# Optimization experiments

Measured on AMD Instinct MI355X. Metric: run time of the kernel, lower is better.

## Reference

```python
import jax, jax.numpy as jnp
import numpy as np

N_NODES = 100000
N_EDGES = 1600000
IN_DIM = 128
HEADS = 8
HEAD_DIM = 16  # output_dim 128 / heads 8
NEG_SLOPE = 0.2  # PyG GATConv default LeakyReLU slope


def setup_inputs() -> dict:
    key = jax.random.key(0)
    k1, k2, k3, k4, k5 = jax.random.split(key, 5)
    x = jax.random.normal(k1, (N_NODES, IN_DIM), dtype=jnp.float32)
    edge_index = jax.random.randint(k2, (2, N_EDGES), 0, N_NODES, dtype=jnp.int64)
    scale = 1.0 / np.sqrt(IN_DIM)
    W = jax.random.normal(k3, (IN_DIM, HEADS * HEAD_DIM), dtype=jnp.float32) * scale
    a_src = jax.random.normal(k4, (HEADS, HEAD_DIM), dtype=jnp.float32) * scale
    a_dst = jax.random.normal(k5, (HEADS, HEAD_DIM), dtype=jnp.float32) * scale
    bias = jnp.zeros((HEADS * HEAD_DIM,), dtype=jnp.float32)
    return {"x": x, "edge_index": edge_index, "W": W, "a_src": a_src, "a_dst": a_dst, "bias": bias}


def reference(x, edge_index, W, a_src, a_dst, bias):
    N = x.shape[0]
    H, D = a_src.shape
    # add self-loops (PyG GATConv default add_self_loops=True)
    loop = jnp.arange(N, dtype=edge_index.dtype)
    src = jnp.concatenate([edge_index[0], loop])  # message sources j
    dst = jnp.concatenate([edge_index[1], loop])  # message targets i

    h = (x @ W).reshape(N, H, D)  # per-head projected features
    alpha_src = jnp.sum(h * a_src, axis=-1)  # [N, H]
    alpha_dst = jnp.sum(h * a_dst, axis=-1)  # [N, H]

    # edge-wise attention logits, softmax over incoming edges of each dst node
    e = jax.nn.leaky_relu(alpha_src[src] + alpha_dst[dst], NEG_SLOPE)  # [E', H]
    e_max = jax.ops.segment_max(e, dst, num_segments=N)
    e_exp = jnp.exp(e - e_max[dst])
    denom = jax.ops.segment_sum(e_exp, dst, num_segments=N)
    alpha = e_exp / (denom[dst] + 1e-16)  # [E', H]

    # weighted scatter-sum of source features
    out = jax.ops.segment_sum(alpha[:, :, None] * h[src], dst, num_segments=N)  # [N, H, D]
    out = out.reshape(N, H * D) + bias
    # wrapper: ReLU (concat=True), dropout is identity in eval mode
    return jax.nn.relu(out)
```

## Files before the change

### kernel.cpp

```cpp
#include <hip/hip_runtime.h>
#include <hip/hip_bf16.h>

#define NEG_SLOPE 0.2f
#define NBUCK 782
#define ABLK 8192
#define CAP 3072

typedef __attribute__((ext_vector_type(8))) short bf16x8v;
typedef __attribute__((ext_vector_type(4))) float f32x4;
typedef __attribute__((ext_vector_type(2))) float f32x2;

__device__ __forceinline__ unsigned f2bf_bits(float f) {
    unsigned u = __float_as_uint(f);
    return (u + 0x7fffu + ((u >> 16) & 1u)) >> 16;
}
__device__ __forceinline__ float bflo(unsigned u) { return __uint_as_float(u << 16); }
__device__ __forceinline__ float bfhi(unsigned u) { return __uint_as_float(u & 0xffff0000u); }

__device__ __forceinline__ void pkfma(f32x2& a, f32x2 x, f32x2 w) {
    asm("v_pk_fma_f32 %0, %1, %2, %0" : "+v"(a) : "v"(x), "v"(w));
}

__global__ __launch_bounds__(256) void gemm_mfma(const float* __restrict__ x,
                                                 const short* __restrict__ WtE,
                                                 short* __restrict__ hout,
                                                 float* __restrict__ as,
                                                 float* __restrict__ ad, int N) {
    __shared__ short xs[64 * 136];
    __shared__ short wt[144 * 136];
    const int tid = threadIdx.x;
    const int r0 = blockIdx.x * 64;

#pragma unroll
    for (int p = 0; p < 9; ++p) {
        int idx = p * 256 + tid;
        int n = idx >> 4, kk = (idx & 15) * 8;
        *(uint4*)&wt[n * 136 + kk] = *(const uint4*)(WtE + n * 128 + kk);
    }
#pragma unroll
    for (int p = 0; p < 8; ++p) {
        int lin = p * 1024 + tid * 4;
        int row = lin >> 7, k = lin & 127;
        int gr = r0 + row;
        int grc = gr < N ? gr : N - 1;
        float4 v = *(const float4*)(x + (size_t)grc * 128 + k);
        unsigned p0 = f2bf_bits(v.x) | (f2bf_bits(v.y) << 16);
        unsigned p1 = f2bf_bits(v.z) | (f2bf_bits(v.w) << 16);
        *(uint2*)&xs[row * 136 + k] = make_uint2(p0, p1);
    }
    __syncthreads();

    const int wv = tid >> 6;
    const int lane = tid & 63;
    const int lc = lane & 15, quad = lane >> 4;
    f32x4 acc[9];
#pragma unroll
    for (int c = 0; c < 9; ++c) acc[c] = (f32x4){0.f, 0.f, 0.f, 0.f};
    const short* aB = &xs[(wv * 16 + lc) * 136 + quad * 8];
    const short* bB = &wt[lc * 136 + quad * 8];
#pragma unroll
    for (int kc = 0; kc < 4; ++kc) {
        bf16x8v af = *(const bf16x8v*)(aB + kc * 32);
#pragma unroll
        for (int c = 0; c < 9; ++c) {
            bf16x8v bf = *(const bf16x8v*)(bB + c * (16 * 136) + kc * 32);
            acc[c] = __builtin_amdgcn_mfma_f32_16x16x32_bf16(af, bf, acc[c], 0, 0, 0);
        }
    }

    const int rowb = r0 + wv * 16 + quad * 4;
#pragma unroll
    for (int c = 0; c < 8; ++c) {
#pragma unroll
        for (int r = 0; r < 4; ++r) {
            int row = rowb + r;
            if (row < N) hout[(size_t)row * 128 + c * 16 + lc] = (short)f2bf_bits(acc[c][r]);
        }
    }
#pragma unroll
    for (int r = 0; r < 4; ++r) {
        int row = rowb + r;
        if (row < N) {
            if (lc < 8) as[row * 8 + lc] = acc[8][r];
            else        ad[row * 8 + (lc - 8)] = acc[8][r];
        }
    }
}

__global__ __launch_bounds__(1024) void bucket_edges(const int* __restrict__ ei, int E,
                                                     int nblk,
                                                     unsigned* __restrict__ slab,
                                                     int2* __restrict__ csG,
                                                     const float* __restrict__ W,
                                                     const float* __restrict__ a_src,
                                                     const float* __restrict__ a_dst,
                                                     short* __restrict__ WtE) {
    const int t = threadIdx.x;
    const int blk = blockIdx.x;

    if (blk >= nblk) {
        int id = (blk - nblk) * 1024 + t;
        if (id < 144 * 128) {
            int n = id >> 7, k = id & 127;
            float v;
            if (n < 128) {
                v = W[k * 128 + n];
            } else if (n < 136) {
                int hh = n - 128; float s = 0.f;
#pragma unroll
                for (int d = 0; d < 16; ++d) s += W[k * 128 + hh * 16 + d] * a_src[hh * 16 + d];
                v = s;
            } else {
                int hh = n - 136; float s = 0.f;
#pragma unroll
                for (int d = 0; d < 16; ++d) s += W[k * 128 + hh * 16 + d] * a_dst[hh * 16 + d];
                v = s;
            }
            WtE[id] = (short)f2bf_bits(v);
        }
        return;
    }

    __shared__ int hist[1024];
    __shared__ int cur[NBUCK];
    __shared__ int wpart[16];
    const int base = blk * ABLK;
    int count = E - base; if (count > ABLK) count = ABLK;

    int sr[8], dr[8];
    hist[t] = 0;
#pragma unroll
    for (int k = 0; k < 8; ++k) {
        int i = k * 1024 + t;
        if (i < count) { sr[k] = ei[base + i]; dr[k] = ei[E + base + i]; }
    }
    __syncthreads();
#pragma unroll
    for (int k = 0; k < 8; ++k) {
        int i = k * 1024 + t;
        if (i < count) atomicAdd(&hist[dr[k] >> 7], 1);
    }
    __syncthreads();
    int v = hist[t];
    int lane = t & 63, wid = t >> 6;
    int sc = v;
#pragma unroll
    for (int off = 1; off < 64; off <<= 1) { int u = __shfl_up(sc, off); if (lane >= off) sc += u; }
    if (lane == 63) wpart[wid] = sc;
    __syncthreads();
    if (wid == 0 && lane < 16) {
        int wv = wpart[lane], wsum = wv;
#pragma unroll
        for (int off = 1; off < 16; off <<= 1) { int u = __shfl_up(wsum, off); if (lane >= off) wsum += u; }
        wpart[lane] = wsum - wv;
    }
    __syncthreads();
    int excl = sc - v + wpart[wid];
    if (t < NBUCK) {
        csG[(size_t)blk * NBUCK + t] = make_int2(v, excl);
        cur[t] = excl;
    }
    __syncthreads();
#pragma unroll
    for (int k = 0; k < 8; ++k) {
        int i = k * 1024 + t;
        if (i < count) {
            int d = dr[k];
            int pos = atomicAdd(&cur[d >> 7], 1);
            slab[(size_t)blk * ABLK + pos] = (unsigned)sr[k] | ((unsigned)(d & 127) << 17);
        }
    }
}

__global__ __launch_bounds__(512) void build_csr(const unsigned* __restrict__ slab,
                                                 const int2* __restrict__ csG,
                                                 int nblk, int N,
                                                 int* __restrict__ rowS,
                                                 int* __restrict__ rowE,
                                                 int* __restrict__ sortedSrc) {
    __shared__ int eL[CAP];
    __shared__ int incl[512];
    __shared__ int cS[512];
    __shared__ int stS[512];
    __shared__ int lp[128];
    __shared__ int wpart[8];
    __shared__ int halfSum;
    const int bb = blockIdx.x;
    const int t = threadIdx.x;
    const int nodeBase = bb << 7;
    const int bBase = bb * CAP;

    int c = 0, st = 0;
    if (t < nblk) { int2 cs = csG[(size_t)t * NBUCK + bb]; c = cs.x; st = cs.y; }
    cS[t] = c; stS[t] = st;
    if (t < 128) lp[t] = 0;
    int lane = t & 63, wid = t >> 6;
    int sc = c;
#pragma unroll
    for (int off = 1; off < 64; off <<= 1) { int u = __shfl_up(sc, off); if (lane >= off) sc += u; }
    if (lane == 63) wpart[wid] = sc;
    __syncthreads();
    if (wid == 0 && lane < 8) {
        int wv = wpart[lane], wsum = wv;
#pragma unroll
        for (int off = 1; off < 8; off <<= 1) { int u = __shfl_up(wsum, off); if (lane >= off) wsum += u; }
        wpart[lane] = wsum - wv;
    }
    __syncthreads();
    incl[t] = sc + wpart[wid];
    __syncthreads();
    int total = incl[511];
    if (total > CAP) total = CAP;
    {
        const int grp = t >> 3, li = t & 7;
        for (int s = grp; s < nblk; s += 64) {
            int cc = cS[s];
            int off0 = incl[s] - cc;
            const unsigned* p = slab + (size_t)s * ABLK + stS[s];
            for (int i = li; i < cc; i += 8) eL[off0 + i] = (int)p[i];
        }
    }
    __syncthreads();
    for (int e = t; e < total; e += 512) atomicAdd(&lp[((unsigned)eL[e]) >> 17], 1);
    __syncthreads();
    int cnt = 0, s2 = 0;
    if (t < 128) {
        cnt = lp[t];
        s2 = cnt;
#pragma unroll
        for (int off = 1; off < 64; off <<= 1) { int u = __shfl_up(s2, off); if (lane >= off) s2 += u; }
        if (t == 63) halfSum = s2;
    }
    __syncthreads();
    if (t < 128) {
        int inc2 = s2 + (t >= 64 ? halfSum : 0);
        int ex = inc2 - cnt;
        int gn = nodeBase + t;
        if (gn < N) { rowS[gn] = bBase + ex; rowE[gn] = bBase + ex + cnt; }
        lp[t] = ex;
    }
    __syncthreads();
    for (int e = t; e < total; e += 512) {
        unsigned pk = (unsigned)eL[e];
        int pos = atomicAdd(&lp[pk >> 17], 1);
        sortedSrc[bBase + pos] = (int)(pk & 0x1FFFFu);
    }
}

__global__ __launch_bounds__(256, 6) void aggregate(const int* __restrict__ rowS,
                                                    const int* __restrict__ rowE,
                                                    const int* __restrict__ sortedSrc,
                                                    const short* __restrict__ h,
                                                    const float* __restrict__ as,
                                                    const float* __restrict__ ad,
                                                    const float* __restrict__ bias,
                                                    float* __restrict__ out, int N) {
    const int wv = __builtin_amdgcn_readfirstlane((int)(threadIdx.x >> 6));
    const int node = blockIdx.x * 4 + wv;
    if (node >= N) return;
    const int lane = threadIdx.x & 63;
    const int g = lane >> 3, p = lane & 7;
    const int start = rowS[node], end = rowE[node];
    const float adv = ad[node * 8 + p];
    const short* hb = h + p * 16;

    f32x2 acc[8];
#pragma unroll
    for (int k = 0; k < 8; ++k) acc[k] = (f32x2){0.f, 0.f};
    float dsum = 0.f;

    float as0 = 0.f, as1 = 0.f, as2 = 0.f;
    uint4 hA0 = {0,0,0,0}, hA1 = {0,0,0,0};
    uint4 hB0 = {0,0,0,0}, hB1 = {0,0,0,0};
    uint4 hC0 = {0,0,0,0}, hC1 = {0,0,0,0};

#define SLOT_LOAD(EV, ASV, H0, H1)                                  \
    if ((EV) < end) {                                               \
        int j = sortedSrc[EV];                                      \
        ASV = as[j * 8 + p];                                        \
        const uint4* hp = (const uint4*)(hb + (size_t)j * 128);     \
        H0 = hp[0]; H1 = hp[1];                                     \
    }

#define EDGE_COMPUTE(ASV, H0, H1)                                   \
    {                                                               \
        float tt = ASV + adv;                                       \
        tt = tt > 0.f ? tt : NEG_SLOPE * tt;                        \
        float w = __expf(tt);                                       \
        f32x2 wp = {w, w};                                          \
        f32x2 tv;                                                   \
        tv.x = bflo(H0.x); tv.y = bfhi(H0.x); pkfma(acc[0], tv, wp); \
        tv.x = bflo(H0.y); tv.y = bfhi(H0.y); pkfma(acc[1], tv, wp); \
        tv.x = bflo(H0.z); tv.y = bfhi(H0.z); pkfma(acc[2], tv, wp); \
        tv.x = bflo(H0.w); tv.y = bfhi(H0.w); pkfma(acc[3], tv, wp); \
        tv.x = bflo(H1.x); tv.y = bfhi(H1.x); pkfma(acc[4], tv, wp); \
        tv.x = bflo(H1.y); tv.y = bfhi(H1.y); pkfma(acc[5], tv, wp); \
        tv.x = bflo(H1.z); tv.y = bfhi(H1.z); pkfma(acc[6], tv, wp); \
        tv.x = bflo(H1.w); tv.y = bfhi(H1.w); pkfma(acc[7], tv, wp); \
        dsum += w;                                                  \
    }

    int e = start + g;
    SLOT_LOAD(e, as0, hA0, hA1)
    SLOT_LOAD(e + 8, as1, hB0, hB1)
    SLOT_LOAD(e + 16, as2, hC0, hC1)

    if (end - start <= 24) {
        if (e < end)      EDGE_COMPUTE(as0, hA0, hA1)
        if (e + 8 < end)  EDGE_COMPUTE(as1, hB0, hB1)
        if (e + 16 < end) EDGE_COMPUTE(as2, hC0, hC1)
    } else {
        while (e < end) {
            EDGE_COMPUTE(as0, hA0, hA1)
            SLOT_LOAD(e + 24, as0, hA0, hA1)
            if (e + 8 < end) EDGE_COMPUTE(as1, hB0, hB1)
            SLOT_LOAD(e + 32, as1, hB0, hB1)
            if (e + 16 < end) EDGE_COMPUTE(as2, hC0, hC1)
            SLOT_LOAD(e + 40, as2, hC0, hC1)
            e += 24;
        }
    }

#pragma unroll
    for (int m = 8; m <= 32; m <<= 1) {
#pragma unroll
        for (int k = 0; k < 8; ++k) {
            acc[k].x += __shfl_xor(acc[k].x, m);
            acc[k].y += __shfl_xor(acc[k].y, m);
        }
        dsum += __shfl_xor(dsum, m);
    }
    {
        float slas = as[node * 8 + p];
        const uint4* hp = (const uint4*)(hb + (size_t)node * 128);
        uint4 s0 = hp[0], s1 = hp[1];
        EDGE_COMPUTE(slas, s0, s1)
    }
    if (g == 0) {
        float inv = 1.0f / (dsum + 1e-16f);
        float* op = out + (size_t)node * 128 + p * 16;
        const float* bp = bias + p * 16;
#pragma unroll
        for (int q = 0; q < 4; ++q) {
            float4 bv = *(const float4*)(bp + q * 4);
            float o0 = acc[2 * q].x     * inv + bv.x;
            float o1 = acc[2 * q].y     * inv + bv.y;
            float o2 = acc[2 * q + 1].x * inv + bv.z;
            float o3 = acc[2 * q + 1].y * inv + bv.w;
            o0 = o0 > 0.f ? o0 : 0.f; o1 = o1 > 0.f ? o1 : 0.f;
            o2 = o2 > 0.f ? o2 : 0.f; o3 = o3 > 0.f ? o3 : 0.f;
            *(float4*)(op + q * 4) = make_float4(o0, o1, o2, o3);
        }
    }
#undef SLOT_LOAD
#undef EDGE_COMPUTE
}

extern "C" void kernel_launch(void* const* d_in, const int* in_sizes, int n_in,
                              void* d_out, int out_size, void* d_ws, size_t ws_size,
                              hipStream_t stream) {
    const float* x     = (const float*)d_in[0];
    const int*   ei    = (const int*)d_in[1];
    const float* W     = (const float*)d_in[2];
    const float* a_src = (const float*)d_in[3];
    const float* a_dst = (const float*)d_in[4];
    const float* bias  = (const float*)d_in[5];
    float* out = (float*)d_out;

    const int N = in_sizes[0] / 128;
    const int E = in_sizes[1] / 2;
    const int nblk = (E + ABLK - 1) / ABLK;

    char* ws = (char*)d_ws;
    size_t off = 0;
    auto alloc = [&](size_t bytes) { void* p = ws + off; off = (off + bytes + 255) & ~(size_t)255; return p; };
    short*    h         = (short*)alloc((size_t)N * 128 * 2);
    float*    as        = (float*)alloc((size_t)N * 8 * 4);
    float*    ad        = (float*)alloc((size_t)N * 8 * 4);
    unsigned* slab      = (unsigned*)alloc((size_t)nblk * ABLK * 4);
    int2*     csG       = (int2*)alloc((size_t)nblk * NBUCK * 8);
    int*      sortedSrc = (int*)alloc((size_t)NBUCK * CAP * 4);
    int*      rowS      = (int*)alloc((size_t)N * 4);
    int*      rowE      = (int*)alloc((size_t)N * 4);
    short*    WtE       = (short*)alloc((size_t)144 * 128 * 2);

    bucket_edges<<<nblk + 18, 1024, 0, stream>>>(ei, E, nblk, slab, csG, W, a_src, a_dst, WtE);
    gemm_mfma<<<(N + 63) / 64, 256, 0, stream>>>(x, WtE, h, as, ad, N);
    build_csr<<<NBUCK, 512, 0, stream>>>(slab, csG, nblk, N, rowS, rowE, sortedSrc);
    aggregate<<<(N + 3) / 4, 256, 0, stream>>>(rowS, rowE, sortedSrc, h, as, ad, bias, out, N);
}
```

Measured before the change: 227.7 us.

## Assign one node per 8-lane group, degree-sorted within each bucket

```diff
diff --git a/kernel.cpp b/kernel.cpp
--- a/kernel.cpp
+++ b/kernel.cpp
@@ -177,12 +177,15 @@
                                                  int nblk, int N,
                                                  int* __restrict__ rowS,
                                                  int* __restrict__ rowE,
-                                                 int* __restrict__ sortedSrc) {
+                                                 int* __restrict__ sortedSrc,
+                                                 int* __restrict__ nodeOrd) {
     __shared__ int eL[CAP];
     __shared__ int incl[512];
     __shared__ int cS[512];
     __shared__ int stS[512];
     __shared__ int lp[128];
+    __shared__ int degS[128];
+    __shared__ int rnk[128];
     __shared__ int wpart[8];
     __shared__ int halfSum;
     const int bb = blockIdx.x;
@@ -193,7 +196,7 @@
     int c = 0, st = 0;
     if (t < nblk) { int2 cs = csG[(size_t)t * NBUCK + bb]; c = cs.x; st = cs.y; }
     cS[t] = c; stS[t] = st;
-    if (t < 128) lp[t] = 0;
+    if (t < 128) { lp[t] = 0; rnk[t] = 0; }
     int lane = t & 63, wid = t >> 6;
     int sc = c;
 #pragma unroll
@@ -226,6 +229,7 @@
     int cnt = 0, s2 = 0;
     if (t < 128) {
         cnt = lp[t];
+        degS[t] = cnt;
         s2 = cnt;
 #pragma unroll
         for (int off = 1; off < 64; off <<= 1) { int u = __shfl_up(s2, off); if (lane >= off) s2 += u; }
@@ -245,23 +249,40 @@
         int pos = atomicAdd(&lp[pk >> 17], 1);
         sortedSrc[bBase + pos] = (int)(pk & 0x1FFFFu);
     }
+    {
+        int n = t & 127, q = t >> 7;
+        int dn = degS[n];
+        int r = 0;
+        int j0 = q * 32;
+#pragma unroll
+        for (int j = 0; j < 32; ++j) {
+            int dj = degS[j0 + j];
+            r += (dj > dn) || (dj == dn && (j0 + j) < n);
+        }
+        atomicAdd(&rnk[n], r);
+    }
+    __syncthreads();
+    if (t < 128) nodeOrd[nodeBase + rnk[t]] = nodeBase + t;
 }
 
 __global__ __launch_bounds__(256, 6) void aggregate(const int* __restrict__ rowS,
                                                     const int* __restrict__ rowE,
                                                     const int* __restrict__ sortedSrc,
+                                                    const int* __restrict__ nodeOrd,
                                                     const short* __restrict__ h,
                                                     const float* __restrict__ as,
                                                     const float* __restrict__ ad,
                                                     const float* __restrict__ bias,
                                                     float* __restrict__ out, int N) {
-    const int wv = __builtin_amdgcn_readfirstlane((int)(threadIdx.x >> 6));
-    const int node = blockIdx.x * 4 + wv;
-    if (node >= N) return;
     const int lane = threadIdx.x & 63;
+    const int wv = threadIdx.x >> 6;
     const int g = lane >> 3, p = lane & 7;
-    const int start = rowS[node], end = rowE[node];
-    const float adv = ad[node * 8 + p];
+    const int slot = blockIdx.x * 32 + wv * 8 + g;
+    const int node = nodeOrd[slot];
+    const bool valid = node < N;
+    int start = 0, end = 0;
+    if (valid) { start = rowS[node]; end = rowE[node]; }
+    const float adv = valid ? ad[node * 8 + p] : 0.f;
     const short* hb = h + p * 16;
 
     f32x2 acc[8];
@@ -300,43 +321,27 @@
         dsum += w;                                                  \
     }
 
-    int e = start + g;
-    SLOT_LOAD(e, as0, hA0, hA1)
-    SLOT_LOAD(e + 8, as1, hB0, hB1)
-    SLOT_LOAD(e + 16, as2, hC0, hC1)
-
-    if (end - start <= 24) {
-        if (e < end)      EDGE_COMPUTE(as0, hA0, hA1)
-        if (e + 8 < end)  EDGE_COMPUTE(as1, hB0, hB1)
-        if (e + 16 < end) EDGE_COMPUTE(as2, hC0, hC1)
-    } else {
-        while (e < end) {
-            EDGE_COMPUTE(as0, hA0, hA1)
-            SLOT_LOAD(e + 24, as0, hA0, hA1)
-            if (e + 8 < end) EDGE_COMPUTE(as1, hB0, hB1)
-            SLOT_LOAD(e + 32, as1, hB0, hB1)
-            if (e + 16 < end) EDGE_COMPUTE(as2, hC0, hC1)
-            SLOT_LOAD(e + 40, as2, hC0, hC1)
-            e += 24;
-        }
-    }
-
-#pragma unroll
-    for (int m = 8; m <= 32; m <<= 1) {
-#pragma unroll
-        for (int k = 0; k < 8; ++k) {
-            acc[k].x += __shfl_xor(acc[k].x, m);
-            acc[k].y += __shfl_xor(acc[k].y, m);
-        }
-        dsum += __shfl_xor(dsum, m);
-    }
-    {
+    int e = start;
+    SLOT_LOAD(e,     as0, hA0, hA1)
+    SLOT_LOAD(e + 1, as1, hB0, hB1)
+    SLOT_LOAD(e + 2, as2, hC0, hC1)
+
+    while (e < end) {
+        EDGE_COMPUTE(as0, hA0, hA1)
+        SLOT_LOAD(e + 3, as0, hA0, hA1)
+        if (e + 1 < end) EDGE_COMPUTE(as1, hB0, hB1)
+        SLOT_LOAD(e + 4, as1, hB0, hB1)
+        if (e + 2 < end) EDGE_COMPUTE(as2, hC0, hC1)
+        SLOT_LOAD(e + 5, as2, hC0, hC1)
+        e += 3;
+    }
+
+    if (valid) {
         float slas = as[node * 8 + p];
         const uint4* hp = (const uint4*)(hb + (size_t)node * 128);
         uint4 s0 = hp[0], s1 = hp[1];
         EDGE_COMPUTE(slas, s0, s1)
-    }
-    if (g == 0) {
+
         float inv = 1.0f / (dsum + 1e-16f);
         float* op = out + (size_t)node * 128 + p * 16;
         const float* bp = bias + p * 16;
@@ -382,10 +387,11 @@
     int*      sortedSrc = (int*)alloc((size_t)NBUCK * CAP * 4);
     int*      rowS      = (int*)alloc((size_t)N * 4);
     int*      rowE      = (int*)alloc((size_t)N * 4);
+    int*      nodeOrd   = (int*)alloc((size_t)NBUCK * 128 * 4);
     short*    WtE       = (short*)alloc((size_t)144 * 128 * 2);
 
     bucket_edges<<<nblk + 18, 1024, 0, stream>>>(ei, E, nblk, slab, csG, W, a_src, a_dst, WtE);
     gemm_mfma<<<(N + 63) / 64, 256, 0, stream>>>(x, WtE, h, as, ad, N);
-    build_csr<<<NBUCK, 512, 0, stream>>>(slab, csG, nblk, N, rowS, rowE, sortedSrc);
-    aggregate<<<(N + 3) / 4, 256, 0, stream>>>(rowS, rowE, sortedSrc, h, as, ad, bias, out, N);
-}
+    build_csr<<<NBUCK, 512, 0, stream>>>(slab, csG, nblk, N, rowS, rowE, sortedSrc, nodeOrd);
+    aggregate<<<(NBUCK * 128) / 32, 256, 0, stream>>>(rowS, rowE, sortedSrc, nodeOrd, h, as, ad, bias, out, N);
+}
```

After: 250.9 us. 1.1x slower.

## Rework aggregate to lane-per-feature-pair with wave-broadcast edge indices

Applied to the files above, without the earlier changes.

```diff
diff --git a/kernel.cpp b/kernel.cpp
--- a/kernel.cpp
+++ b/kernel.cpp
@@ -8,7 +8,6 @@
 
 typedef __attribute__((ext_vector_type(8))) short bf16x8v;
 typedef __attribute__((ext_vector_type(4))) float f32x4;
-typedef __attribute__((ext_vector_type(2))) float f32x2;
 
 __device__ __forceinline__ unsigned f2bf_bits(float f) {
     unsigned u = __float_as_uint(f);
@@ -16,10 +15,6 @@
 }
 __device__ __forceinline__ float bflo(unsigned u) { return __uint_as_float(u << 16); }
 __device__ __forceinline__ float bfhi(unsigned u) { return __uint_as_float(u & 0xffff0000u); }
-
-__device__ __forceinline__ void pkfma(f32x2& a, f32x2 x, f32x2 w) {
-    asm("v_pk_fma_f32 %0, %1, %2, %0" : "+v"(a) : "v"(x), "v"(w));
-}
 
 __global__ __launch_bounds__(256) void gemm_mfma(const float* __restrict__ x,
                                                  const short* __restrict__ WtE,
@@ -247,7 +242,7 @@
     }
 }
 
-__global__ __launch_bounds__(256, 6) void aggregate(const int* __restrict__ rowS,
+__global__ __launch_bounds__(256, 8) void aggregate(const int* __restrict__ rowS,
                                                     const int* __restrict__ rowE,
                                                     const int* __restrict__ sortedSrc,
                                                     const short* __restrict__ h,
@@ -255,105 +250,65 @@
                                                     const float* __restrict__ ad,
                                                     const float* __restrict__ bias,
                                                     float* __restrict__ out, int N) {
-    const int wv = __builtin_amdgcn_readfirstlane((int)(threadIdx.x >> 6));
-    const int node = blockIdx.x * 4 + wv;
+    const int lane = threadIdx.x & 63;
+    const int wv = threadIdx.x >> 6;
+    const int node = __builtin_amdgcn_readfirstlane(blockIdx.x * 4 + wv);
     if (node >= N) return;
-    const int lane = threadIdx.x & 63;
-    const int g = lane >> 3, p = lane & 7;
-    const int start = rowS[node], end = rowE[node];
+    const int p = lane >> 3;
+    const int start = __builtin_amdgcn_readfirstlane(rowS[node]);
+    const int end   = __builtin_amdgcn_readfirstlane(rowE[node]);
     const float adv = ad[node * 8 + p];
-    const short* hb = h + p * 16;
-
-    f32x2 acc[8];
-#pragma unroll
-    for (int k = 0; k < 8; ++k) acc[k] = (f32x2){0.f, 0.f};
+
+    float accx = 0.f, accy = 0.f;
     float dsum = 0.f;
 
-    float as0 = 0.f, as1 = 0.f, as2 = 0.f;
-    uint4 hA0 = {0,0,0,0}, hA1 = {0,0,0,0};
-    uint4 hB0 = {0,0,0,0}, hB1 = {0,0,0,0};
-    uint4 hC0 = {0,0,0,0}, hC1 = {0,0,0,0};
-
-#define SLOT_LOAD(EV, ASV, H0, H1)                                  \
-    if ((EV) < end) {                                               \
-        int j = sortedSrc[EV];                                      \
-        ASV = as[j * 8 + p];                                        \
-        const uint4* hp = (const uint4*)(hb + (size_t)j * 128);     \
-        H0 = hp[0]; H1 = hp[1];                                     \
-    }
-
-#define EDGE_COMPUTE(ASV, H0, H1)                                   \
-    {                                                               \
-        float tt = ASV + adv;                                       \
-        tt = tt > 0.f ? tt : NEG_SLOPE * tt;                        \
-        float w = __expf(tt);                                       \
-        f32x2 wp = {w, w};                                          \
-        f32x2 tv;                                                   \
-        tv.x = bflo(H0.x); tv.y = bfhi(H0.x); pkfma(acc[0], tv, wp); \
-        tv.x = bflo(H0.y); tv.y = bfhi(H0.y); pkfma(acc[1], tv, wp); \
-        tv.x = bflo(H0.z); tv.y = bfhi(H0.z); pkfma(acc[2], tv, wp); \
-        tv.x = bflo(H0.w); tv.y = bfhi(H0.w); pkfma(acc[3], tv, wp); \
-        tv.x = bflo(H1.x); tv.y = bfhi(H1.x); pkfma(acc[4], tv, wp); \
-        tv.x = bflo(H1.y); tv.y = bfhi(H1.y); pkfma(acc[5], tv, wp); \
-        tv.x = bflo(H1.z); tv.y = bfhi(H1.z); pkfma(acc[6], tv, wp); \
-        tv.x = bflo(H1.w); tv.y = bfhi(H1.w); pkfma(acc[7], tv, wp); \
-        dsum += w;                                                  \
-    }
-
-    int e = start + g;
-    SLOT_LOAD(e, as0, hA0, hA1)
-    SLOT_LOAD(e + 8, as1, hB0, hB1)
-    SLOT_LOAD(e + 16, as2, hC0, hC1)
-
-    if (end - start <= 24) {
-        if (e < end)      EDGE_COMPUTE(as0, hA0, hA1)
-        if (e + 8 < end)  EDGE_COMPUTE(as1, hB0, hB1)
-        if (e + 16 < end) EDGE_COMPUTE(as2, hC0, hC1)
-    } else {
-        while (e < end) {
-            EDGE_COMPUTE(as0, hA0, hA1)
-            SLOT_LOAD(e + 24, as0, hA0, hA1)
-            if (e + 8 < end) EDGE_COMPUTE(as1, hB0, hB1)
-            SLOT_LOAD(e + 32, as1, hB0, hB1)
-            if (e + 16 < end) EDGE_COMPUTE(as2, hC0, hC1)
-            SLOT_LOAD(e + 40, as2, hC0, hC1)
-            e += 24;
-        }
-    }
-
-#pragma unroll
-    for (int m = 8; m <= 32; m <<= 1) {
+    int e = start;
+    int iv = node;
+    { int q = e + (lane & 7); if (q < end) iv = sortedSrc[q]; }
+
+    while (e < end) {
+        float asv[8]; unsigned hwv[8];
 #pragma unroll
         for (int k = 0; k < 8; ++k) {
-            acc[k].x += __shfl_xor(acc[k].x, m);
-            acc[k].y += __shfl_xor(acc[k].y, m);
-        }
-        dsum += __shfl_xor(dsum, m);
-    }
+            int j = __builtin_amdgcn_readlane(iv, k);
+            asv[k] = as[j * 8 + p];
+            hwv[k] = *(const unsigned*)(h + (size_t)j * 128 + lane * 2);
+        }
+        int en = e + 8;
+        int iv2 = node;
+        { int q = en + (lane & 7); if (q < end) iv2 = sortedSrc[q]; }
+#pragma unroll
+        for (int k = 0; k < 8; ++k) {
+            if (e + k < end) {
+                float tt = asv[k] + adv;
+                tt = tt > 0.f ? tt : NEG_SLOPE * tt;
+                float w = __expf(tt);
+                unsigned u = hwv[k];
+                accx += w * bflo(u);
+                accy += w * bfhi(u);
+                dsum += w;
+            }
+        }
+        iv = iv2; e = en;
+    }
+
     {
-        float slas = as[node * 8 + p];
-        const uint4* hp = (const uint4*)(hb + (size_t)node * 128);
-        uint4 s0 = hp[0], s1 = hp[1];
-        EDGE_COMPUTE(slas, s0, s1)
-    }
-    if (g == 0) {
-        float inv = 1.0f / (dsum + 1e-16f);
-        float* op = out + (size_t)node * 128 + p * 16;
-        const float* bp = bias + p * 16;
-#pragma unroll
-        for (int q = 0; q < 4; ++q) {
-            float4 bv = *(const float4*)(bp + q * 4);
-            float o0 = acc[2 * q].x     * inv + bv.x;
-            float o1 = acc[2 * q].y     * inv + bv.y;
-            float o2 = acc[2 * q + 1].x * inv + bv.z;
-            float o3 = acc[2 * q + 1].y * inv + bv.w;
-            o0 = o0 > 0.f ? o0 : 0.f; o1 = o1 > 0.f ? o1 : 0.f;
-            o2 = o2 > 0.f ? o2 : 0.f; o3 = o3 > 0.f ? o3 : 0.f;
-            *(float4*)(op + q * 4) = make_float4(o0, o1, o2, o3);
-        }
-    }
-#undef SLOT_LOAD
-#undef EDGE_COMPUTE
+        float tt = as[node * 8 + p] + adv;
+        tt = tt > 0.f ? tt : NEG_SLOPE * tt;
+        float w = __expf(tt);
+        unsigned u = *(const unsigned*)(h + (size_t)node * 128 + lane * 2);
+        accx += w * bflo(u);
+        accy += w * bfhi(u);
+        dsum += w;
+    }
+
+    float inv = 1.0f / (dsum + 1e-16f);
+    float2 bv = *(const float2*)(bias + lane * 2);
+    float o0 = accx * inv + bv.x;
+    float o1 = accy * inv + bv.y;
+    o0 = o0 > 0.f ? o0 : 0.f;
+    o1 = o1 > 0.f ? o1 : 0.f;
+    *(float2*)(out + (size_t)node * 128 + lane * 2) = make_float2(o0, o1);
 }
 
 extern "C" void kernel_launch(void* const* d_in, const int* in_sizes, int n_in,
```

Result: faster. 222.9 us (median of 2 runs) (-2.1%).
